# Performance work log

Measured on AMD Instinct MI355X. Metric: run time of the kernel, lower is better.

## Reference

```python
import jax, jax.numpy as jnp
import numpy as np

B, T, D = 2, 2048, 2048
H, HD = 16, 128
ROPE_BASE = 10000.0
EPS = 1e-6


def setup_inputs() -> dict:
    key = jax.random.key(0)
    ks = jax.random.split(key, 5)
    s = 1.0 / np.sqrt(D)
    return {
        "x": jax.random.normal(ks[0], (B, T, D), dtype=jnp.float32),
        "Wq": jax.random.normal(ks[1], (H * HD, D), dtype=jnp.float32) * s,
        "Wk": jax.random.normal(ks[2], (H * HD, D), dtype=jnp.float32) * s,
        "Wv": jax.random.normal(ks[3], (H * HD, D), dtype=jnp.float32) * s,
        "Wo": jax.random.normal(ks[4], (D, H * HD), dtype=jnp.float32) * s,
        "q_norm_w": jnp.ones((HD,), dtype=jnp.float32),
        "k_norm_w": jnp.ones((HD,), dtype=jnp.float32),
    }


def _rms_norm(x, w):
    # RMSNorm over last dim, no centering (LLaMA/Qwen style)
    norm = jnp.sqrt(jnp.mean(jnp.square(x), axis=-1, keepdims=True) + EPS)
    return x / norm * w


def _rope_interleaved(x):
    # x: (B, T, H, HD); GPT-NeoX interleaved style, sequential positions
    dim = HD // 2
    freqs = jnp.exp(-jnp.arange(0, dim, dtype=jnp.float32) * jnp.log(ROPE_BASE) / dim)
    angles = jnp.arange(T, dtype=jnp.float32)[:, None] * freqs[None, :]  # (T, dim)
    cos = jnp.cos(angles)[None, :, None, :]  # (1, T, 1, dim)
    sin = jnp.sin(angles)[None, :, None, :]
    x_even = x[..., ::2]
    x_odd = x[..., 1::2]
    r_even = x_even * cos - x_odd * sin
    r_odd = x_even * sin + x_odd * cos
    return jnp.stack([r_even, r_odd], axis=-1).reshape(x.shape)


def reference(x, Wq, Wk, Wv, Wo, q_norm_w, k_norm_w):
    # QKV projections (weights stored [out, in], per llm_linear einsum)
    q = jnp.einsum("btd,od->bto", x, Wq).reshape(B, T, H, HD)
    k = jnp.einsum("btd,od->bto", x, Wk).reshape(B, T, H, HD)
    v = jnp.einsum("btd,od->bto", x, Wv).reshape(B, T, H, HD)
    # per-head QK RMSNorm
    q = _rms_norm(q, q_norm_w)
    k = _rms_norm(k, k_norm_w)
    # rotary embeddings
    q = _rope_interleaved(q)
    k = _rope_interleaved(k)
    # causal scaled dot-product attention
    scale = 1.0 / jnp.sqrt(jnp.asarray(HD, dtype=x.dtype))
    scores = jnp.einsum("bthd,bshd->bhts", q, k) * scale  # (B, H, T, T)
    causal = jnp.tril(jnp.ones((T, T), dtype=bool))
    scores = jnp.where(causal[None, None, :, :], scores, jnp.asarray(-1e30, dtype=scores.dtype))
    probs = jax.nn.softmax(scores, axis=-1)
    ctx = jnp.einsum("bhts,bshd->bthd", probs, v).reshape(B, T, H * HD)
    # output projection
    return jnp.einsum("bto,do->btd", ctx, Wo)
```

## Files before the change

### kernel.cpp

```cpp
#include <hip/hip_runtime.h>
#include <cstdint>
#include <cstddef>

#define B_ 2
#define T_ 2048
#define D_ 2048
#define H_ 16
#define HD_ 128
#define EPS_ 1e-6f
#define QSCALE_ 0.08838834764831845f
#define KVSTRIDE_ (H_ * HD_)

typedef unsigned short u16;
typedef short s16x8 __attribute__((ext_vector_type(8)));
typedef float f32x4 __attribute__((ext_vector_type(4)));

__device__ __forceinline__ float bf2f(u16 h) {
  union { unsigned int u; float f; } v;
  v.u = ((unsigned int)h) << 16;
  return v.f;
}
__device__ __forceinline__ u16 f2bf(float f) {
  union { float f; unsigned int u; } v;
  v.f = f;
  unsigned int r = v.u + 0x7FFFu + ((v.u >> 16) & 1u);
  return (u16)(r >> 16);
}

__device__ __forceinline__ void gload16(const void* g, void* l) {
  __builtin_amdgcn_global_load_lds(
      (const __attribute__((address_space(1))) unsigned int*)g,
      (__attribute__((address_space(3))) unsigned int*)l, 16, 0, 0);
}

__global__ void cvt_all(const float* __restrict__ x, const float* __restrict__ Wq,
                        const float* __restrict__ Wk, const float* __restrict__ Wv,
                        const float* __restrict__ Wo, u16* __restrict__ xb,
                        u16* __restrict__ wqkb, u16* __restrict__ wvb, u16* __restrict__ wob,
                        float2* __restrict__ rope) {
  const int XQ = 2097152, WQ = 1048576, CAST_END = XQ + 4 * WQ;
  int i = blockIdx.x * blockDim.x + threadIdx.x;
  if (i >= CAST_END) {
    int idx = i - CAST_END;
    if (idx < T_ * 64) {
      int t = idx >> 6, fi = idx & 63;
      float freq = expf(-(float)fi * (9.210340371976184f / 64.0f));
      float ang = (float)t * freq;
      float sn, cs;
      sincosf(ang, &sn, &cs);
      rope[idx] = make_float2(cs, sn);
    }
    return;
  }
  const float* src;
  u16* dst;
  int off;
  if (i < XQ) { src = x; dst = xb; off = i; }
  else if (i < XQ + WQ) { src = Wq; dst = wqkb; off = i - XQ; }
  else if (i < XQ + 2 * WQ) { src = Wk; dst = wqkb + (size_t)WQ * 4; off = i - XQ - WQ; }
  else if (i < XQ + 3 * WQ) { src = Wv; dst = wvb; off = i - XQ - 2 * WQ; }
  else { src = Wo; dst = wob; off = i - XQ - 3 * WQ; }
  float4 v = ((const float4*)src)[off];
  ((ushort4*)dst)[off] = make_ushort4(f2bf(v.x), f2bf(v.y), f2bf(v.z), f2bf(v.w));
}

template <int MODE>
__global__ __launch_bounds__(256, 2) void gemm_btn(const u16* __restrict__ A,
                                                   const u16* __restrict__ Bm,
                                                   void* __restrict__ Cout,
                                                   void* __restrict__ Cout2,
                                                   int M, int N, int K) {
  __shared__ u16 As[2][2 * 128 * 32];
  __shared__ u16 Bs[2][2 * 128 * 32];
  const int tid = threadIdx.x;
  const int w = tid >> 6, lane = tid & 63, quad = lane >> 4, c = lane & 15;
  const int wm = w & 1, wn = w >> 1;
  const int m0 = blockIdx.y * 128, n0 = blockIdx.x * 128;
  const int NT = K >> 6;

  f32x4 acc[4][4];
#pragma unroll
  for (int i = 0; i < 4; ++i)
#pragma unroll
    for (int j = 0; j < 4; ++j) acc[i][j] = (f32x4){0.f, 0.f, 0.f, 0.f};

  auto STAGE = [&](int t, int buf) {
    int k0 = t << 6;
#pragma unroll
    for (int i = 0; i < 4; ++i) {
      int chunk = (w * 4 + i) * 64 + lane;
      int kc = chunk >> 9;
      int within = chunk & 511;
      int row = within >> 2, cc = within & 3;
      gload16(A + (size_t)(m0 + row) * K + k0 + kc * 32 + cc * 8, (void*)(&As[buf][0] + chunk * 8));
      gload16(Bm + (size_t)(n0 + row) * K + k0 + kc * 32 + cc * 8, (void*)(&Bs[buf][0] + chunk * 8));
    }
  };

  STAGE(0, 0);
  STAGE(1, 1);
  asm volatile("s_waitcnt vmcnt(8)" ::: "memory");
  __builtin_amdgcn_s_barrier();

  for (int t = 0; t < NT; ++t) {
    const int cur = t & 1;
    s16x8 af[4][2], bf[4][2];
#pragma unroll
    for (int kc = 0; kc < 2; ++kc) {
#pragma unroll
      for (int mi = 0; mi < 4; ++mi)
        af[mi][kc] = *(const s16x8*)(&As[cur][0] + kc * 4096 + (wm * 64 + mi * 16 + c) * 32 + quad * 8);
#pragma unroll
      for (int ni = 0; ni < 4; ++ni)
        bf[ni][kc] = *(const s16x8*)(&Bs[cur][0] + kc * 4096 + (wn * 64 + ni * 16 + c) * 32 + quad * 8);
    }
    asm volatile("s_waitcnt lgkmcnt(0)" ::: "memory");
    __builtin_amdgcn_s_barrier();
    if (t + 2 < NT) STAGE(t + 2, cur);

#pragma unroll
    for (int kc = 0; kc < 2; ++kc)
#pragma unroll
      for (int mi = 0; mi < 4; ++mi)
#pragma unroll
        for (int ni = 0; ni < 4; ++ni)
          acc[mi][ni] = __builtin_amdgcn_mfma_f32_16x16x32_bf16(af[mi][kc], bf[ni][kc], acc[mi][ni], 0, 0, 0);

    if (t + 1 < NT) {
      if (t + 2 < NT)
        asm volatile("s_waitcnt vmcnt(8)" ::: "memory");
      else
        asm volatile("s_waitcnt vmcnt(0)" ::: "memory");
      __builtin_amdgcn_s_barrier();
    }
  }

  u16* dst16 = (u16*)Cout;
  int coloff = 0, nstride = N;
  if (MODE == 2) {
    nstride = 2048;
    if (n0 >= 2048) { dst16 = (u16*)Cout2; coloff = -2048; }
  }
#pragma unroll
  for (int mi = 0; mi < 4; ++mi)
#pragma unroll
    for (int ni = 0; ni < 4; ++ni)
#pragma unroll
      for (int r = 0; r < 4; ++r) {
        int row = m0 + wm * 64 + mi * 16 + quad * 4 + r;
        int col = n0 + wn * 64 + ni * 16 + c + coloff;
        float v = acc[mi][ni][r];
        if (MODE == 0)
          ((float*)Cout)[(size_t)row * N + col] = v;
        else
          dst16[(size_t)row * nstride + col] = f2bf(v);
      }
}

__global__ void rmsnorm_rope_k(u16* __restrict__ kx, const float* __restrict__ kw,
                               const float2* __restrict__ rope) {
  const int tid = threadIdx.x;
  const int w = tid >> 6, lane = tid & 63;
  const int vec = blockIdx.x * 4 + w;
  const int t = (vec >> 4) & (T_ - 1);
  u16* base = kx + (size_t)vec * HD_;
  unsigned int pk = *(const unsigned int*)(base + lane * 2);
  float e = bf2f((u16)(pk & 0xFFFFu));
  float o = bf2f((u16)(pk >> 16));
  float ss = e * e + o * o;
#pragma unroll
  for (int off = 1; off < 64; off <<= 1) ss += __shfl_xor(ss, off, 64);
  float rn = rsqrtf(ss * (1.0f / HD_) + EPS_);
  float we = kw[lane * 2], wo = kw[lane * 2 + 1];
  e = e * rn * we;
  o = o * rn * wo;
  float2 cn = rope[t * 64 + lane];
  float re = e * cn.x - o * cn.y;
  float ro = e * cn.y + o * cn.x;
  *(unsigned int*)(base + lane * 2) = ((unsigned int)f2bf(ro) << 16) | (unsigned int)f2bf(re);
}

__global__ __launch_bounds__(256, 2) void attn_fwd(const u16* __restrict__ Q,
                                                   const u16* __restrict__ Kg,
                                                   const u16* __restrict__ Vt,
                                                   u16* __restrict__ O,
                                                   const float* __restrict__ qw,
                                                   const float2* __restrict__ rope) {
  __shared__ u16 Ks[2][64 * 128];
  __shared__ u16 Vts[2][128 * 64];
  __shared__ u16 Ps[64 * 64];
  const int tid = threadIdx.x;
  const int w = tid >> 6, lane = tid & 63, quad = lane >> 4, c = lane & 15;
  const int c7 = (c & 7) * 8;
  const int bid = blockIdx.x;
  const int qt = 31 - (bid >> 5);
  const int h = bid & 15;
  const int b = (bid >> 4) & 1;
  const int q0 = qt * 64;

  const int trow = q0 + w * 16 + c;
  const u16* qbase = Q + ((size_t)(b * T_ + trow) * H_ + h) * HD_;
  s16x8 qraw[4];
#pragma unroll
  for (int kk = 0; kk < 4; ++kk) qraw[kk] = *(const s16x8*)(qbase + kk * 32 + quad * 8);
  float qv[4][8];
  float ss = 0.f;
#pragma unroll
  for (int kk = 0; kk < 4; ++kk)
#pragma unroll
    for (int e = 0; e < 8; ++e) {
      float v = bf2f((u16)qraw[kk][e]);
      qv[kk][e] = v;
      ss += v * v;
    }
  ss += __shfl_xor(ss, 16, 64);
  ss += __shfl_xor(ss, 32, 64);
  float rn = rsqrtf(ss * (1.0f / HD_) + EPS_);
  const float2* rrow = rope + trow * 64;
  const float2* qw2 = (const float2*)qw;
  s16x8 qf[4];
#pragma unroll
  for (int kk = 0; kk < 4; ++kk) {
    const float4* rp = (const float4*)(rrow + kk * 16 + quad * 4);
    float4 cs0 = rp[0];
    float4 cs1 = rp[1];
    float cosv[4] = {cs0.x, cs0.z, cs1.x, cs1.z};
    float sinv[4] = {cs0.y, cs0.w, cs1.y, cs1.w};
#pragma unroll
    for (int p = 0; p < 4; ++p) {
      int idx = kk * 32 + quad * 8 + 2 * p;
      float2 wv = qw2[idx >> 1];
      float e0 = qv[kk][2 * p] * rn * wv.x;
      float o0 = qv[kk][2 * p + 1] * rn * wv.y;
      qf[kk][2 * p] = (short)f2bf((e0 * cosv[p] - o0 * sinv[p]) * QSCALE_);
      qf[kk][2 * p + 1] = (short)f2bf((e0 * sinv[p] + o0 * cosv[p]) * QSCALE_);
    }
  }

  f32x4 of[8];
#pragma unroll
  for (int i = 0; i < 8; ++i) of[i] = (f32x4){0.f, 0.f, 0.f, 0.f};
  float m_i[4] = {-1e30f, -1e30f, -1e30f, -1e30f};
  float lp[4] = {0.f, 0.f, 0.f, 0.f};

  const u16* kbase = Kg + ((size_t)b * T_ * H_ + h) * HD_;
  const u16* vtbase = Vt + (size_t)(h * HD_) * (B_ * T_) + (size_t)b * T_;

  auto STAGE = [&](int j, int buf) {
    const u16* krow = kbase + (size_t)(j * 64) * KVSTRIDE_;
    const u16* vrow = vtbase + j * 64;
#pragma unroll
    for (int i = 0; i < 4; ++i) {
      int chunk = i * 256 + tid;
      int krowi = chunk >> 4, kslot = (chunk & 15) ^ (krowi & 7);
      gload16(krow + (size_t)krowi * KVSTRIDE_ + kslot * 8, (void*)(&Ks[buf][0] + chunk * 8));
      int vrowi = chunk >> 3, vslot = (chunk & 7) ^ (vrowi & 7);
      gload16(vrow + (size_t)vrowi * (B_ * T_) + vslot * 8, (void*)(&Vts[buf][0] + chunk * 8));
    }
  };

  STAGE(0, 0);
  __syncthreads();
  int cur = 0;

  for (int j = 0; j <= qt; ++j) {
    if (j < qt) STAGE(j + 1, cur ^ 1);

    f32x4 sf[4];
#pragma unroll
    for (int ni = 0; ni < 4; ++ni) {
      f32x4 a = (f32x4){0.f, 0.f, 0.f, 0.f};
#pragma unroll
      for (int kk = 0; kk < 4; ++kk) {
        s16x8 bfr = *(const s16x8*)(&Ks[cur][(ni * 16 + c) * 128 + ((kk * 32 + quad * 8) ^ c7)]);
        a = __builtin_amdgcn_mfma_f32_16x16x32_bf16(qf[kk], bfr, a, 0, 0, 0);
      }
      sf[ni] = a;
    }
    if (j == qt) {
#pragma unroll
      for (int ni = 0; ni < 4; ++ni)
#pragma unroll
        for (int r = 0; r < 4; ++r) {
          int rowg = w * 16 + quad * 4 + r;
          int colg = ni * 16 + c;
          if (colg > rowg) sf[ni][r] = -1e30f;
        }
    }
    float mc[4];
#pragma unroll
    for (int r = 0; r < 4; ++r)
      mc[r] = fmaxf(fmaxf(sf[0][r], sf[1][r]), fmaxf(sf[2][r], sf[3][r]));
#pragma unroll
    for (int off = 1; off < 16; off <<= 1)
#pragma unroll
      for (int r = 0; r < 4; ++r) mc[r] = fmaxf(mc[r], __shfl_xor(mc[r], off, 64));
#pragma unroll
    for (int r = 0; r < 4; ++r) {
      float mnew = fmaxf(m_i[r], mc[r]);
      float alpha = __expf(m_i[r] - mnew);
      m_i[r] = mnew;
      lp[r] *= alpha;
#pragma unroll
      for (int ot = 0; ot < 8; ++ot) of[ot][r] *= alpha;
    }
#pragma unroll
    for (int ni = 0; ni < 4; ++ni)
#pragma unroll
      for (int r = 0; r < 4; ++r) {
        float p = __expf(sf[ni][r] - m_i[r]);
        sf[ni][r] = p;
        lp[r] += p;
      }
#pragma unroll
    for (int ni = 0; ni < 4; ++ni)
#pragma unroll
      for (int r = 0; r < 4; ++r) {
        int row = w * 16 + quad * 4 + r;
        Ps[row * 64 + ((ni * 16 + c) ^ ((row & 7) * 8))] = f2bf(sf[ni][r]);
      }
    s16x8 pa[2];
    pa[0] = *(const s16x8*)(&Ps[(w * 16 + c) * 64 + ((quad * 8) ^ c7)]);
    pa[1] = *(const s16x8*)(&Ps[(w * 16 + c) * 64 + ((32 + quad * 8) ^ c7)]);
#pragma unroll
    for (int ot = 0; ot < 8; ++ot) {
#pragma unroll
      for (int kk = 0; kk < 2; ++kk) {
        s16x8 vfr = *(const s16x8*)(&Vts[cur][(ot * 16 + c) * 64 + ((kk * 32 + quad * 8) ^ c7)]);
        of[ot] = __builtin_amdgcn_mfma_f32_16x16x32_bf16(pa[kk], vfr, of[ot], 0, 0, 0);
      }
    }

    __syncthreads();
    cur ^= 1;
  }

#pragma unroll
  for (int off = 1; off < 16; off <<= 1)
#pragma unroll
    for (int r = 0; r < 4; ++r) lp[r] += __shfl_xor(lp[r], off, 64);
  float inv[4];
#pragma unroll
  for (int r = 0; r < 4; ++r) inv[r] = 1.0f / lp[r];
  u16* obase = O + ((size_t)(b * T_ + q0) * H_ + h) * HD_;
#pragma unroll
  for (int ot = 0; ot < 8; ++ot)
#pragma unroll
    for (int r = 0; r < 4; ++r)
      obase[(size_t)(w * 16 + quad * 4 + r) * KVSTRIDE_ + ot * 16 + c] = f2bf(of[ot][r] * inv[r]);
}

extern "C" void kernel_launch(void* const* d_in, const int* in_sizes, int n_in,
                              void* d_out, int out_size, void* d_ws, size_t ws_size,
                              hipStream_t stream) {
  const float* x = (const float*)d_in[0];
  const float* Wq = (const float*)d_in[1];
  const float* Wk = (const float*)d_in[2];
  const float* Wv = (const float*)d_in[3];
  const float* Wo = (const float*)d_in[4];
  const float* qw = (const float*)d_in[5];
  const float* kw = (const float*)d_in[6];
  float* out = (float*)d_out;

  const size_t xE = (size_t)B_ * T_ * D_;
  const size_t wE = (size_t)D_ * H_ * HD_;
  const size_t ropeB = (size_t)T_ * 64 * sizeof(float2);
  const size_t need = xE * 2 * 5 + wE * 2 * 4 + ropeB;
  if (ws_size < need) return;

  char* ws = (char*)d_ws;
  u16* xb = (u16*)ws;    ws += xE * 2;
  u16* wqkb = (u16*)ws;  ws += wE * 2 * 2;
  u16* wvb = (u16*)ws;   ws += wE * 2;
  u16* wob = (u16*)ws;   ws += wE * 2;
  u16* qb = (u16*)ws;    ws += xE * 2;
  u16* kb = (u16*)ws;    ws += xE * 2;
  u16* vtb = (u16*)ws;   ws += xE * 2;
  u16* ctxb = (u16*)ws;  ws += xE * 2;
  float2* rope = (float2*)ws; ws += ropeB;

  cvt_all<<<25088, 256, 0, stream>>>(x, Wq, Wk, Wv, Wo, xb, wqkb, wvb, wob, rope);

  dim3 gqk(32, 32);
  gemm_btn<2><<<gqk, 256, 0, stream>>>(xb, wqkb, qb, kb, 4096, 4096, 2048);
  dim3 ggv(32, 16);
  gemm_btn<1><<<ggv, 256, 0, stream>>>(wvb, xb, vtb, nullptr, 2048, 4096, 2048);

  rmsnorm_rope_k<<<16384, 256, 0, stream>>>(kb, kw, rope);

  attn_fwd<<<B_ * H_ * (T_ / 64), 256, 0, stream>>>(qb, kb, vtb, ctxb, qw, rope);

  dim3 gg(16, 32);
  gemm_btn<0><<<gg, 256, 0, stream>>>(ctxb, wob, out, nullptr, 4096, 2048, 2048);
}
```

Baseline: 374.0 us.

## Fuse QKV GEMMs and fold QK RMSNorm+RoPE into GEMM epilogue

Merges the Q/K GEMM and the transposed V GEMM into one launch using a combined grid, and moves per-head RMSNorm, RoPE and the Q scaling into that GEMM's epilogue. A cross-wave shared-memory reduction produces the per-row sum of squares over each 128-wide head tile. This removes the separate K norm/rope kernel, one launch, and the Q normalization prologue inside attention. In exchange the epilogue gains shuffles, an extra barrier and scattered bf16 stores.

```diff
diff --git a/kernel.cpp b/kernel.cpp
--- a/kernel.cpp
+++ b/kernel.cpp
@@ -64,11 +64,156 @@
   ((ushort4*)dst)[off] = make_ushort4(f2bf(v.x), f2bf(v.y), f2bf(v.z), f2bf(v.w));
 }
 
-template <int MODE>
+__global__ __launch_bounds__(256, 2) void gemm_qkv(const u16* __restrict__ xb,
+                                                   const u16* __restrict__ wqkb,
+                                                   const u16* __restrict__ wvb,
+                                                   u16* __restrict__ qb, u16* __restrict__ kb,
+                                                   u16* __restrict__ vtb,
+                                                   const float* __restrict__ qw,
+                                                   const float* __restrict__ kw,
+                                                   const float2* __restrict__ rope) {
+  __shared__ u16 As[2][2 * 128 * 32];
+  __shared__ u16 Bs[2][2 * 128 * 32];
+  const int tid = threadIdx.x;
+  const int w = tid >> 6, lane = tid & 63, quad = lane >> 4, c = lane & 15;
+  const int wm = w & 1, wn = w >> 1;
+  const bool isV = blockIdx.y >= 32;
+  const u16* A = isV ? wvb : xb;
+  const u16* Bm = isV ? xb : wqkb;
+  const int m0 = (isV ? (blockIdx.y - 32) : blockIdx.y) * 128;
+  const int n0 = blockIdx.x * 128;
+  const int K = 2048, NT = 32;
+
+  f32x4 acc[4][4];
+#pragma unroll
+  for (int i = 0; i < 4; ++i)
+#pragma unroll
+    for (int j = 0; j < 4; ++j) acc[i][j] = (f32x4){0.f, 0.f, 0.f, 0.f};
+
+  auto STAGE = [&](int t, int buf) {
+    int k0 = t << 6;
+#pragma unroll
+    for (int i = 0; i < 4; ++i) {
+      int chunk = (w * 4 + i) * 64 + lane;
+      int kc = chunk >> 9;
+      int within = chunk & 511;
+      int row = within >> 2, cc = within & 3;
+      gload16(A + (size_t)(m0 + row) * K + k0 + kc * 32 + cc * 8, (void*)(&As[buf][0] + chunk * 8));
+      gload16(Bm + (size_t)(n0 + row) * K + k0 + kc * 32 + cc * 8, (void*)(&Bs[buf][0] + chunk * 8));
+    }
+  };
+
+  STAGE(0, 0);
+  STAGE(1, 1);
+  asm volatile("s_waitcnt vmcnt(8)" ::: "memory");
+  __builtin_amdgcn_s_barrier();
+
+  for (int t = 0; t < NT; ++t) {
+    const int cur = t & 1;
+    s16x8 af[4][2], bf[4][2];
+#pragma unroll
+    for (int kc = 0; kc < 2; ++kc) {
+#pragma unroll
+      for (int mi = 0; mi < 4; ++mi)
+        af[mi][kc] = *(const s16x8*)(&As[cur][0] + kc * 4096 + (wm * 64 + mi * 16 + c) * 32 + quad * 8);
+#pragma unroll
+      for (int ni = 0; ni < 4; ++ni)
+        bf[ni][kc] = *(const s16x8*)(&Bs[cur][0] + kc * 4096 + (wn * 64 + ni * 16 + c) * 32 + quad * 8);
+    }
+    asm volatile("s_waitcnt lgkmcnt(0)" ::: "memory");
+    __builtin_amdgcn_s_barrier();
+    if (t + 2 < NT) STAGE(t + 2, cur);
+
+#pragma unroll
+    for (int kc = 0; kc < 2; ++kc)
+#pragma unroll
+      for (int mi = 0; mi < 4; ++mi)
+#pragma unroll
+        for (int ni = 0; ni < 4; ++ni)
+          acc[mi][ni] = __builtin_amdgcn_mfma_f32_16x16x32_bf16(af[mi][kc], bf[ni][kc], acc[mi][ni], 0, 0, 0);
+
+    if (t + 1 < NT) {
+      if (t + 2 < NT)
+        asm volatile("s_waitcnt vmcnt(8)" ::: "memory");
+      else
+        asm volatile("s_waitcnt vmcnt(0)" ::: "memory");
+      __builtin_amdgcn_s_barrier();
+    }
+  }
+
+  if (isV) {
+#pragma unroll
+    for (int mi = 0; mi < 4; ++mi)
+#pragma unroll
+      for (int ni = 0; ni < 4; ++ni)
+#pragma unroll
+        for (int r = 0; r < 4; ++r) {
+          int row = m0 + wm * 64 + mi * 16 + quad * 4 + r;
+          int col = n0 + wn * 64 + ni * 16 + c;
+          vtb[(size_t)row * 4096 + col] = f2bf(acc[mi][ni][r]);
+        }
+    return;
+  }
+
+  float p[4][4];
+#pragma unroll
+  for (int mi = 0; mi < 4; ++mi)
+#pragma unroll
+    for (int r = 0; r < 4; ++r) {
+      float s = 0.f;
+#pragma unroll
+      for (int ni = 0; ni < 4; ++ni) s += acc[mi][ni][r] * acc[mi][ni][r];
+      p[mi][r] = s;
+    }
+#pragma unroll
+  for (int off = 1; off < 16; off <<= 1)
+#pragma unroll
+    for (int mi = 0; mi < 4; ++mi)
+#pragma unroll
+      for (int r = 0; r < 4; ++r) p[mi][r] += __shfl_xor(p[mi][r], off, 64);
+  float* ssred = (float*)&As[0][0];
+  if (c == 0) {
+#pragma unroll
+    for (int mi = 0; mi < 4; ++mi)
+#pragma unroll
+      for (int r = 0; r < 4; ++r)
+        ssred[wn * 128 + wm * 64 + mi * 16 + quad * 4 + r] = p[mi][r];
+  }
+  __syncthreads();
+  float rn_[4][4];
+#pragma unroll
+  for (int mi = 0; mi < 4; ++mi)
+#pragma unroll
+    for (int r = 0; r < 4; ++r) {
+      int lr = wm * 64 + mi * 16 + quad * 4 + r;
+      rn_[mi][r] = rsqrtf((ssred[lr] + ssred[128 + lr]) * (1.0f / HD_) + EPS_);
+    }
+  const bool isQ = (n0 < 2048);
+  const float* nw = isQ ? qw : kw;
+  const float scl = isQ ? QSCALE_ : 1.0f;
+  u16* dst = isQ ? qb : kb;
+  const int nbase = n0 - (isQ ? 0 : 2048);
+#pragma unroll
+  for (int mi = 0; mi < 4; ++mi)
+#pragma unroll
+    for (int ni = 0; ni < 4; ++ni)
+#pragma unroll
+      for (int r = 0; r < 4; ++r) {
+        int row = m0 + wm * 64 + mi * 16 + quad * 4 + r;
+        int t = row & (T_ - 1);
+        int col = nbase + wn * 64 + ni * 16 + c;
+        int d = col & 127;
+        float vn = acc[mi][ni][r] * rn_[mi][r] * nw[d];
+        float partner = __shfl_xor(vn, 1, 64);
+        float2 cn = rope[t * 64 + (d >> 1)];
+        float res = (c & 1) ? (partner * cn.y + vn * cn.x) : (vn * cn.x - partner * cn.y);
+        dst[(size_t)row * 2048 + col] = f2bf(res * scl);
+      }
+}
+
 __global__ __launch_bounds__(256, 2) void gemm_btn(const u16* __restrict__ A,
                                                    const u16* __restrict__ Bm,
-                                                   void* __restrict__ Cout,
-                                                   void* __restrict__ Cout2,
+                                                   float* __restrict__ Cout,
                                                    int M, int N, int K) {
   __shared__ u16 As[2][2 * 128 * 32];
   __shared__ u16 Bs[2][2 * 128 * 32];
@@ -135,12 +280,6 @@
     }
   }
 
-  u16* dst16 = (u16*)Cout;
-  int coloff = 0, nstride = N;
-  if (MODE == 2) {
-    nstride = 2048;
-    if (n0 >= 2048) { dst16 = (u16*)Cout2; coloff = -2048; }
-  }
 #pragma unroll
   for (int mi = 0; mi < 4; ++mi)
 #pragma unroll
@@ -148,44 +287,15 @@
 #pragma unroll
       for (int r = 0; r < 4; ++r) {
         int row = m0 + wm * 64 + mi * 16 + quad * 4 + r;
-        int col = n0 + wn * 64 + ni * 16 + c + coloff;
-        float v = acc[mi][ni][r];
-        if (MODE == 0)
-          ((float*)Cout)[(size_t)row * N + col] = v;
-        else
-          dst16[(size_t)row * nstride + col] = f2bf(v);
-      }
-}
-
-__global__ void rmsnorm_rope_k(u16* __restrict__ kx, const float* __restrict__ kw,
-                               const float2* __restrict__ rope) {
-  const int tid = threadIdx.x;
-  const int w = tid >> 6, lane = tid & 63;
-  const int vec = blockIdx.x * 4 + w;
-  const int t = (vec >> 4) & (T_ - 1);
-  u16* base = kx + (size_t)vec * HD_;
-  unsigned int pk = *(const unsigned int*)(base + lane * 2);
-  float e = bf2f((u16)(pk & 0xFFFFu));
-  float o = bf2f((u16)(pk >> 16));
-  float ss = e * e + o * o;
-#pragma unroll
-  for (int off = 1; off < 64; off <<= 1) ss += __shfl_xor(ss, off, 64);
-  float rn = rsqrtf(ss * (1.0f / HD_) + EPS_);
-  float we = kw[lane * 2], wo = kw[lane * 2 + 1];
-  e = e * rn * we;
-  o = o * rn * wo;
-  float2 cn = rope[t * 64 + lane];
-  float re = e * cn.x - o * cn.y;
-  float ro = e * cn.y + o * cn.x;
-  *(unsigned int*)(base + lane * 2) = ((unsigned int)f2bf(ro) << 16) | (unsigned int)f2bf(re);
+        int col = n0 + wn * 64 + ni * 16 + c;
+        Cout[(size_t)row * N + col] = acc[mi][ni][r];
+      }
 }
 
 __global__ __launch_bounds__(256, 2) void attn_fwd(const u16* __restrict__ Q,
                                                    const u16* __restrict__ Kg,
                                                    const u16* __restrict__ Vt,
-                                                   u16* __restrict__ O,
-                                                   const float* __restrict__ qw,
-                                                   const float2* __restrict__ rope) {
+                                                   u16* __restrict__ O) {
   __shared__ u16 Ks[2][64 * 128];
   __shared__ u16 Vts[2][128 * 64];
   __shared__ u16 Ps[64 * 64];
@@ -198,44 +308,10 @@
   const int b = (bid >> 4) & 1;
   const int q0 = qt * 64;
 
-  const int trow = q0 + w * 16 + c;
-  const u16* qbase = Q + ((size_t)(b * T_ + trow) * H_ + h) * HD_;
-  s16x8 qraw[4];
-#pragma unroll
-  for (int kk = 0; kk < 4; ++kk) qraw[kk] = *(const s16x8*)(qbase + kk * 32 + quad * 8);
-  float qv[4][8];
-  float ss = 0.f;
-#pragma unroll
-  for (int kk = 0; kk < 4; ++kk)
-#pragma unroll
-    for (int e = 0; e < 8; ++e) {
-      float v = bf2f((u16)qraw[kk][e]);
-      qv[kk][e] = v;
-      ss += v * v;
-    }
-  ss += __shfl_xor(ss, 16, 64);
-  ss += __shfl_xor(ss, 32, 64);
-  float rn = rsqrtf(ss * (1.0f / HD_) + EPS_);
-  const float2* rrow = rope + trow * 64;
-  const float2* qw2 = (const float2*)qw;
   s16x8 qf[4];
-#pragma unroll
-  for (int kk = 0; kk < 4; ++kk) {
-    const float4* rp = (const float4*)(rrow + kk * 16 + quad * 4);
-    float4 cs0 = rp[0];
-    float4 cs1 = rp[1];
-    float cosv[4] = {cs0.x, cs0.z, cs1.x, cs1.z};
-    float sinv[4] = {cs0.y, cs0.w, cs1.y, cs1.w};
-#pragma unroll
-    for (int p = 0; p < 4; ++p) {
-      int idx = kk * 32 + quad * 8 + 2 * p;
-      float2 wv = qw2[idx >> 1];
-      float e0 = qv[kk][2 * p] * rn * wv.x;
-      float o0 = qv[kk][2 * p + 1] * rn * wv.y;
-      qf[kk][2 * p] = (short)f2bf((e0 * cosv[p] - o0 * sinv[p]) * QSCALE_);
-      qf[kk][2 * p + 1] = (short)f2bf((e0 * sinv[p] + o0 * cosv[p]) * QSCALE_);
-    }
-  }
+  const u16* qbase = Q + ((size_t)(b * T_ + q0 + w * 16 + c) * H_ + h) * HD_;
+#pragma unroll
+  for (int kk = 0; kk < 4; ++kk) qf[kk] = *(const s16x8*)(qbase + kk * 32 + quad * 8);
 
   f32x4 of[8];
 #pragma unroll
@@ -381,15 +457,11 @@
 
   cvt_all<<<25088, 256, 0, stream>>>(x, Wq, Wk, Wv, Wo, xb, wqkb, wvb, wob, rope);
 
-  dim3 gqk(32, 32);
-  gemm_btn<2><<<gqk, 256, 0, stream>>>(xb, wqkb, qb, kb, 4096, 4096, 2048);
-  dim3 ggv(32, 16);
-  gemm_btn<1><<<ggv, 256, 0, stream>>>(wvb, xb, vtb, nullptr, 2048, 4096, 2048);
-
-  rmsnorm_rope_k<<<16384, 256, 0, stream>>>(kb, kw, rope);
-
-  attn_fwd<<<B_ * H_ * (T_ / 64), 256, 0, stream>>>(qb, kb, vtb, ctxb, qw, rope);
+  dim3 gqkv(32, 48);
+  gemm_qkv<<<gqkv, 256, 0, stream>>>(xb, wqkb, wvb, qb, kb, vtb, qw, kw, rope);
+
+  attn_fwd<<<B_ * H_ * (T_ / 64), 256, 0, stream>>>(qb, kb, vtb, ctxb);
 
   dim3 gg(16, 32);
-  gemm_btn<0><<<gg, 256, 0, stream>>>(ctxb, wob, out, nullptr, 4096, 2048, 2048);
-}
+  gemm_btn<<<gg, 256, 0, stream>>>(ctxb, wob, out, 4096, 2048, 2048);
+}
```

Measured after the change: 360.5 us. 1.04x faster.
